# Performance work log

Measured on AMD Instinct MI355X. Metric: run time of the kernel, lower is better.

Reference implementation:

```python
import jax, jax.numpy as jnp
import numpy as np
import math

NUM_HEADS = 32
NUM_KV_HEADS = 8
HEAD_DIM = 128
ROPE_THETA = 10000.0


def _rope_cos_sin(position_ids, head_dim, dtype):
    # inv_freq: [head_dim/2]
    inv_freq = 1.0 / (ROPE_THETA ** (jnp.arange(0, head_dim, 2, dtype=jnp.float32) / head_dim))
    # freqs: [B, S, head_dim/2]
    freqs = position_ids.astype(jnp.float32)[:, :, None] * inv_freq[None, None, :]
    emb = jnp.concatenate([freqs, freqs], axis=-1)  # [B, S, head_dim]
    return jnp.cos(emb).astype(dtype), jnp.sin(emb).astype(dtype)


def _rotate_half(x):
    h = x.shape[-1] // 2
    return jnp.concatenate([-x[..., h:], x[..., :h]], axis=-1)


def setup_inputs() -> dict:
    key = jax.random.key(0)
    ks = jax.random.split(key, 5)
    B, S, H = 1, 2048, 4096
    kv_dim = NUM_KV_HEADS * HEAD_DIM
    return {
        "hidden_states": jax.random.normal(ks[0], (B, S, H), dtype=jnp.float32),
        "position_ids": jnp.arange(S, dtype=jnp.int64 if jax.config.jax_enable_x64 else jnp.int32)[None, :].repeat(B, axis=0),
        "Wq": jax.random.normal(ks[1], (H, H), dtype=jnp.float32) * 0.02,
        "Wk": jax.random.normal(ks[2], (kv_dim, H), dtype=jnp.float32) * 0.02,
        "Wv": jax.random.normal(ks[3], (kv_dim, H), dtype=jnp.float32) * 0.02,
        "Wo": jax.random.normal(ks[4], (H, H), dtype=jnp.float32) * 0.02,
    }


def reference(hidden_states, position_ids, Wq, Wk, Wv, Wo):
    B, S, H = hidden_states.shape
    groups = NUM_HEADS // NUM_KV_HEADS

    # QKV projections (nn.Linear: x @ W.T, no bias)
    q = (hidden_states @ Wq.T).reshape(B, S, NUM_HEADS, HEAD_DIM).transpose(0, 2, 1, 3)
    k = (hidden_states @ Wk.T).reshape(B, S, NUM_KV_HEADS, HEAD_DIM).transpose(0, 2, 1, 3)
    v = (hidden_states @ Wv.T).reshape(B, S, NUM_KV_HEADS, HEAD_DIM).transpose(0, 2, 1, 3)

    # RoPE
    cos, sin = _rope_cos_sin(position_ids, HEAD_DIM, q.dtype)
    cos = cos[:, None, :, :]  # [B,1,S,hd]
    sin = sin[:, None, :, :]
    q = q * cos + _rotate_half(q) * sin
    k = k * cos + _rotate_half(k) * sin

    # repeat_kv: expand KV heads to match Q heads
    k = jnp.repeat(k, groups, axis=1)  # [B, NUM_HEADS, S, hd]
    v = jnp.repeat(v, groups, axis=1)

    # scores + causal mask + fp32 softmax
    scores = jnp.einsum("bhqd,bhkd->bhqk", q, k) / math.sqrt(HEAD_DIM)
    causal = jnp.tril(jnp.ones((S, S), dtype=bool))
    scores = jnp.where(causal[None, None, :, :], scores, jnp.finfo(jnp.float32).min)
    attn = jax.nn.softmax(scores.astype(jnp.float32), axis=-1).astype(q.dtype)

    # attention output + output projection
    out = jnp.einsum("bhqk,bhkd->bhqd", attn, v)
    out = out.transpose(0, 2, 1, 3).reshape(B, S, H)
    return out @ Wo.T
```

## Files before the change

kernel.cpp:

```cpp
#include <hip/hip_runtime.h>
#include <stdint.h>


typedef __attribute__((ext_vector_type(8))) __bf16 bf16x8;
typedef __attribute__((ext_vector_type(4))) float floatx4;

#define S_LEN 2048
#define HID   4096
#define NH    32
#define NKV   8
#define HD    128

__device__ __forceinline__ unsigned short f2bf(float f) {
  union { float f; uint32_t u; } v; v.f = f;
  return (unsigned short)((v.u + 0x7fffu + ((v.u >> 16) & 1u)) >> 16);
}

__device__ __forceinline__ void gload_lds16(const unsigned short* g, unsigned short* l) {
  __builtin_amdgcn_global_load_lds(
      (const __attribute__((address_space(1))) void*)g,
      (__attribute__((address_space(3))) void*)l,
      16, 0, 0);
}

__global__ void cast_bf16_kernel(const float* __restrict__ in,
                                 unsigned short* __restrict__ out, int n4) {
  int i = blockIdx.x * blockDim.x + threadIdx.x;
  if (i >= n4) return;
  float4 f = ((const float4*)in)[i];
  ushort4 o = make_ushort4(f2bf(f.x), f2bf(f.y), f2bf(f.z), f2bf(f.w));
  ((ushort4*)out)[i] = o;
}

#define GT 32

__device__ __forceinline__ void read_frag4(
    bf16x8* f, const unsigned short* S, int row0, int l15, int quad) {
#pragma unroll
  for (int i = 0; i < 4; ++i) {
    const int row = row0 + i * 16 + l15;
    f[i] = *(const bf16x8*)&S[row * GT + (((quad ^ (row >> 1)) & 3) * 8)];
  }
}

__device__ __forceinline__ void mfma_c8(
    const bf16x8* a, const bf16x8* b, floatx4 acc[8][4], int mi0) {
#pragma unroll
  for (int mi = 0; mi < 2; ++mi)
#pragma unroll
    for (int ni = 0; ni < 4; ++ni)
      acc[mi0 + mi][ni] = __builtin_amdgcn_mfma_f32_16x16x32_bf16(
          a[mi], b[ni], acc[mi0 + mi][ni], 0, 0, 0);
}

__global__ __launch_bounds__(512, 2) void gemm_bt256_kernel(
    const unsigned short* __restrict__ A,
    const unsigned short* __restrict__ B,
    float* __restrict__ C, int M, int N, int K) {
  __shared__ unsigned short As[4][256 * GT];
  __shared__ unsigned short Bs[4][256 * GT];
  const int m0 = blockIdx.y * 256;
  const int n0 = blockIdx.x * 256;
  const int tid = threadIdx.x;
  const int lane = tid & 63;
  const int wv = tid >> 6;
  const int wr = wv >> 2;
  const int wc = wv & 3;
  const int l15 = lane & 15;
  const int quad = lane >> 4;

  const int ch0 = wv * 64 + lane;
  const int ch1 = ch0 + 512;
  const int cs0 = ch0 ^ ((ch0 >> 3) & 3);
  const int cs1 = ch1 ^ ((ch1 >> 3) & 3);
  const int r0s = cs0 >> 2, c0s = (cs0 & 3) * 8;
  const int r1s = cs1 >> 2, c1s = (cs1 & 3) * 8;

  floatx4 acc[8][4];
#pragma unroll
  for (int i = 0; i < 8; i++)
#pragma unroll
    for (int j = 0; j < 4; j++) acc[i][j] = (floatx4){0.f, 0.f, 0.f, 0.f};

  const int T = K / GT;

#define STAGE_T(kk0, s)                                                        \
  do {                                                                         \
    gload_lds16(A + (size_t)(m0 + r0s) * K + (kk0) + c0s, &As[s][ch0 * 8]);    \
    gload_lds16(A + (size_t)(m0 + r1s) * K + (kk0) + c1s, &As[s][ch1 * 8]);    \
    gload_lds16(B + (size_t)(n0 + r0s) * K + (kk0) + c0s, &Bs[s][ch0 * 8]);    \
    gload_lds16(B + (size_t)(n0 + r1s) * K + (kk0) + c1s, &Bs[s][ch1 * 8]);    \
  } while (0)

  STAGE_T(0, 0);
  STAGE_T(GT, 1);
  STAGE_T(2 * GT, 2);
  asm volatile("s_waitcnt vmcnt(4)" ::: "memory");
  __builtin_amdgcn_s_barrier();

  bf16x8 fA[12], fB[12];
  read_frag4(fA + 0, As[0], wr * 128, l15, quad);
  read_frag4(fA + 4, As[0], wr * 128 + 64, l15, quad);
  read_frag4(fA + 8, Bs[0], wc * 64, l15, quad);
  asm volatile("s_waitcnt lgkmcnt(0)" ::: "memory");
  __builtin_amdgcn_sched_barrier(0);

#define MCLUSTER(CUR, mi0)                                                     \
  __builtin_amdgcn_sched_barrier(0);                                           \
  __builtin_amdgcn_s_setprio(1);                                               \
  mfma_c8((CUR) + (mi0), (CUR) + 8, acc, (mi0));                               \
  __builtin_amdgcn_s_setprio(0);                                               \
  __builtin_amdgcn_sched_barrier(0);

#define BODY(tt, CUR, NXT)                                                     \
  do {                                                                         \
    const int t_ = (tt);                                                       \
    const int sl_ = (t_ + 1) & 3;                                              \
    const bool rd_ = (t_ + 1 < T);                                             \
    if (rd_) read_frag4((NXT) + 0, As[sl_], wr * 128, l15, quad);              \
    MCLUSTER(CUR, 0)                                                           \
    if (rd_) read_frag4((NXT) + 4, As[sl_], wr * 128 + 64, l15, quad);         \
    MCLUSTER(CUR, 2)                                                           \
    if (rd_) read_frag4((NXT) + 8, Bs[sl_], wc * 64, l15, quad);               \
    MCLUSTER(CUR, 4)                                                           \
    if (t_ + 3 < T) STAGE_T((t_ + 3) * GT, (t_ + 3) & 3);                      \
    MCLUSTER(CUR, 6)                                                           \
    asm volatile("s_waitcnt lgkmcnt(0)" ::: "memory");                         \
                  \
    if (t_ + 3 < T)      { asm volatile("s_waitcnt vmcnt(4)" ::: "memory"); }  \
    else if (t_ + 2 < T) { asm volatile("s_waitcnt vmcnt(0)" ::: "memory"); }  \
    __builtin_amdgcn_sched_barrier(0);                                         \
    __builtin_amdgcn_s_barrier();                                              \
  } while (0)

  for (int t = 0; t < T; t += 2) {
    BODY(t, fA, fB);
    BODY(t + 1, fB, fA);
  }
#undef BODY
#undef MCLUSTER
#undef STAGE_T

#pragma unroll
  for (int mi = 0; mi < 8; ++mi) {
    const int row = m0 + wr * 128 + mi * 16 + quad * 4;
#pragma unroll
    for (int ni = 0; ni < 4; ++ni) {
      const int col = n0 + wc * 64 + ni * 16 + l15;
#pragma unroll
      for (int r = 0; r < 4; ++r)
        C[(size_t)(row + r) * N + col] = acc[mi][ni][r];
    }
  }
}

#define BM 128
#define BN 128
#define BK 32

__global__ __launch_bounds__(256) void gemm_bt_kernel(
    const unsigned short* __restrict__ A,
    const unsigned short* __restrict__ B,
    float* __restrict__ C, int M, int N, int K) {
  __shared__ unsigned short As[BM * BK];
  __shared__ unsigned short Bs[BN * BK];
  const int m0 = blockIdx.y * BM;
  const int n0 = blockIdx.x * BN;
  const int tid = threadIdx.x;
  const int lane = tid & 63;
  const int l15 = lane & 15;
  const int quad = lane >> 4;
  const int w = tid >> 6;
  const int wm = (w >> 1) * 64;
  const int wn = (w & 1) * 64;

  floatx4 acc[4][4];
#pragma unroll
  for (int i = 0; i < 4; i++)
#pragma unroll
    for (int j = 0; j < 4; j++) acc[i][j] = (floatx4){0.f, 0.f, 0.f, 0.f};

  const int c0 = tid, c1 = tid + 256;
  const int r0 = c0 >> 2, o0 = (c0 & 3) * 8;
  const int r1 = c1 >> 2, o1 = (c1 & 3) * 8;

  for (int k0 = 0; k0 < K; k0 += BK) {
    __syncthreads();
    gload_lds16(A + (size_t)(m0 + r0) * K + k0 + o0, As + c0 * 8);
    gload_lds16(A + (size_t)(m0 + r1) * K + k0 + o1, As + c1 * 8);
    gload_lds16(B + (size_t)(n0 + r0) * K + k0 + o0, Bs + c0 * 8);
    gload_lds16(B + (size_t)(n0 + r1) * K + k0 + o1, Bs + c1 * 8);
    __syncthreads();

    bf16x8 a_frag[4], b_frag[4];
#pragma unroll
    for (int mt = 0; mt < 4; mt++)
      a_frag[mt] = *(const bf16x8*)&As[(wm + mt * 16 + l15) * BK + quad * 8];
#pragma unroll
    for (int nt = 0; nt < 4; nt++)
      b_frag[nt] = *(const bf16x8*)&Bs[(wn + nt * 16 + l15) * BK + quad * 8];
#pragma unroll
    for (int mt = 0; mt < 4; mt++)
#pragma unroll
      for (int nt = 0; nt < 4; nt++)
        acc[mt][nt] = __builtin_amdgcn_mfma_f32_16x16x32_bf16(
            a_frag[mt], b_frag[nt], acc[mt][nt], 0, 0, 0);
  }

#pragma unroll
  for (int mt = 0; mt < 4; mt++) {
#pragma unroll
    for (int nt = 0; nt < 4; nt++) {
      const int row = m0 + wm + mt * 16 + quad * 4;
      const int col = n0 + wn + nt * 16 + l15;
#pragma unroll
      for (int r = 0; r < 4; r++)
        C[(size_t)(row + r) * N + col] = acc[mt][nt][r];
    }
  }
}

__global__ void rope_kernel(const float* __restrict__ Cqkv,
                            const int* __restrict__ pos_ids,
                            unsigned short* __restrict__ Qb,
                            unsigned short* __restrict__ Kb) {
  int t = blockIdx.x * blockDim.x + threadIdx.x;
  int j = t & 63;
  int s = t >> 6;
  int hh = blockIdx.y;
  float pos = (float)pos_ids[s];
  float ang = pos * exp2f(-0.20762050593045222f * (float)j);
  float c = cosf(ang), sn = sinf(ang);
  if (hh < NH) {
    const float* row = Cqkv + (size_t)s * 6144 + hh * HD;
    float x1 = row[j], x2 = row[j + 64];
    unsigned short* q = Qb + ((size_t)hh * S_LEN + s) * HD;
    q[j]      = f2bf(x1 * c - x2 * sn);
    q[j + 64] = f2bf(x2 * c + x1 * sn);
  } else {
    int kh = hh - NH;
    const float* row = Cqkv + (size_t)s * 6144 + HID + kh * HD;
    float x1 = row[j], x2 = row[j + 64];
    unsigned short* k = Kb + ((size_t)kh * S_LEN + s) * HD;
    k[j]      = f2bf(x1 * c - x2 * sn);
    k[j + 64] = f2bf(x2 * c + x1 * sn);
  }
}

__global__ void vtrans_kernel(const float* __restrict__ Cqkv,
                              unsigned short* __restrict__ Vt) {
  int t = blockIdx.x * blockDim.x + threadIdx.x;
  int s = t & (S_LEN - 1);
  int d = (t >> 11) & (HD - 1);
  int kh = t >> 18;
  Vt[((size_t)kh * HD + d) * S_LEN + s] =
      f2bf(Cqkv[(size_t)s * 6144 + (HID + NKV * HD) + kh * HD + d]);
}

__global__ __launch_bounds__(256, 2) void flash_attn_kernel(
    const unsigned short* __restrict__ Qb, const unsigned short* __restrict__ Kb,
    const unsigned short* __restrict__ Vt, unsigned short* __restrict__ O) {
  __shared__ unsigned short Ks[2][64 * 128];
  __shared__ unsigned short Vs[2][128 * 64];
  __shared__ unsigned short Ps[4][2][16 * 64];
  const int qb = gridDim.x - 1 - blockIdx.x;
  const int q0 = qb * 128;
  const int h = blockIdx.y;
  const int kvh = h >> 2;
  const int tid = threadIdx.x;
  const int lane = tid & 63;
  const int w = tid >> 6;
  const int l15 = lane & 15;
  const int quad = lane >> 4;
  const int qlo = q0 + w * 32;

  const unsigned short* Qh = Qb + (size_t)h * S_LEN * HD;
  const unsigned short* Kh = Kb + (size_t)kvh * S_LEN * HD;
  const unsigned short* Vh = Vt + (size_t)kvh * HD * S_LEN;

  const int nkt = q0 / 64 + 2;

#pragma unroll
  for (int it = 0; it < 4; it++) {
    int c = tid + it * 256;
    int kr = c >> 4, kj = (c & 15) ^ (kr & 15);
    gload_lds16(Kh + (size_t)kr * HD + kj * 8, Ks[0] + c * 8);
    int vd = c >> 3, vj = (c & 7) ^ (vd & 7);
    gload_lds16(Vh + (size_t)vd * S_LEN + vj * 8, Vs[0] + c * 8);
  }

  bf16x8 q_frag[2][4];
#pragma unroll
  for (int mf = 0; mf < 2; mf++)
#pragma unroll
    for (int kk = 0; kk < 4; kk++)
      q_frag[mf][kk] = *(const bf16x8*)&Qh[(size_t)(qlo + mf * 16 + l15) * HD + kk * 32 + quad * 8];

  bf16x8 ones_frag;
  {
    union { unsigned short u; __bf16 b; } ov;
    ov.u = (l15 == 0) ? 0x3F80 : 0;
#pragma unroll
    for (int j = 0; j < 8; j++) ones_frag[j] = ov.b;
  }

  floatx4 o_acc[2][8];
  floatx4 o_l[2];
#pragma unroll
  for (int mf = 0; mf < 2; mf++) {
#pragma unroll
    for (int i = 0; i < 8; i++) o_acc[mf][i] = (floatx4){0.f, 0.f, 0.f, 0.f};
    o_l[mf] = (floatx4){0.f, 0.f, 0.f, 0.f};
  }
  const float SC2 = 0.12751738f;

  for (int kt = 0; kt < nkt; kt++) {
    const int kbase = kt * 64;
    const int buf = kt & 1;
    __syncthreads();

    if (kt + 1 < nkt) {
      const int kb2 = kbase + 64;
#pragma unroll
      for (int it = 0; it < 4; it++) {
        int c = tid + it * 256;
        int kr = c >> 4, kj = (c & 15) ^ (kr & 15);
        gload_lds16(Kh + (size_t)(kb2 + kr) * HD + kj * 8, Ks[buf ^ 1] + c * 8);
        int vd = c >> 3, vj = (c & 7) ^ (vd & 7);
        gload_lds16(Vh + (size_t)vd * S_LEN + kb2 + vj * 8, Vs[buf ^ 1] + c * 8);
      }
    }

    if (kbase <= qlo + 31) {
      floatx4 s_acc[2][4];
#pragma unroll
      for (int mf = 0; mf < 2; mf++)
#pragma unroll
        for (int nt = 0; nt < 4; nt++) s_acc[mf][nt] = (floatx4){0.f, 0.f, 0.f, 0.f};
#pragma unroll
      for (int kk = 0; kk < 4; kk++)
#pragma unroll
        for (int nt = 0; nt < 4; nt++) {
          bf16x8 k_frag = *(const bf16x8*)&Ks[buf][(nt * 16 + l15) * 128 + (((kk * 4 + quad) ^ l15) * 8)];
#pragma unroll
          for (int mf = 0; mf < 2; mf++)
            s_acc[mf][nt] = __builtin_amdgcn_mfma_f32_16x16x32_bf16(
                q_frag[mf][kk], k_frag, s_acc[mf][nt], 0, 0, 0);
        }

      const bool diag = (kbase + 63 > qlo);
#pragma unroll
      for (int mf = 0; mf < 2; mf++) {
#pragma unroll
        for (int nt = 0; nt < 4; nt++) {
          int kc = kbase + nt * 16 + l15;
          int qrow = qlo + mf * 16 + quad * 4;
          int chunk2 = nt * 2 + (l15 >> 3);
          int coff = l15 & 7;
#pragma unroll
          for (int r = 0; r < 4; r++) {
            float pv = exp2f(s_acc[mf][nt][r] * SC2);
            if (diag && kc > qrow + r) pv = 0.f;
            int row = quad * 4 + r;
            Ps[w][mf][row * 64 + ((chunk2 ^ (row & 7)) * 8) + coff] = f2bf(pv);
          }
        }
      }

#pragma unroll
      for (int kk2 = 0; kk2 < 2; kk2++) {
        bf16x8 p_frag[2];
#pragma unroll
        for (int mf = 0; mf < 2; mf++)
          p_frag[mf] = *(const bf16x8*)&Ps[w][mf][l15 * 64 + (((kk2 * 4 + quad) ^ (l15 & 7)) * 8)];
#pragma unroll
        for (int dt = 0; dt < 8; dt++) {
          bf16x8 v_frag = *(const bf16x8*)&Vs[buf][(dt * 16 + l15) * 64 + (((kk2 * 4 + quad) ^ (l15 & 7)) * 8)];
#pragma unroll
          for (int mf = 0; mf < 2; mf++)
            o_acc[mf][dt] = __builtin_amdgcn_mfma_f32_16x16x32_bf16(
                p_frag[mf], v_frag, o_acc[mf][dt], 0, 0, 0);
        }
#pragma unroll
        for (int mf = 0; mf < 2; mf++)
          o_l[mf] = __builtin_amdgcn_mfma_f32_16x16x32_bf16(
              p_frag[mf], ones_frag, o_l[mf], 0, 0, 0);
      }
    }
  }

#pragma unroll
  for (int mf = 0; mf < 2; mf++)
#pragma unroll
    for (int r = 0; r < 4; r++) {
      float lsum = __shfl(o_l[mf][r], lane & 48, 64);
      float inv = 1.f / lsum;
      int qr = qlo + mf * 16 + quad * 4 + r;
#pragma unroll
      for (int dt = 0; dt < 8; dt++)
        O[(size_t)qr * HID + h * HD + dt * 16 + l15] = f2bf(o_acc[mf][dt][r] * inv);
    }
}

extern "C" void kernel_launch(void* const* d_in, const int* in_sizes, int n_in,
                              void* d_out, int out_size, void* d_ws, size_t ws_size,
                              hipStream_t stream) {
  const float* hidden = (const float*)d_in[0];
  const int*   pos    = (const int*)d_in[1];
  const float* Wq     = (const float*)d_in[2];
  const float* Wk     = (const float*)d_in[3];
  const float* Wv     = (const float*)d_in[4];
  const float* Wo     = (const float*)d_in[5];

  char* ws = (char*)d_ws;
  size_t off = 0;
  unsigned short* h_b    = (unsigned short*)(ws + off); off += (size_t)S_LEN * HID * 2;
  unsigned short* Wqkv_b = (unsigned short*)(ws + off); off += (size_t)6144 * HID * 2;
  unsigned short* Wo_b   = (unsigned short*)(ws + off); off += (size_t)HID * HID * 2;
  float*          Cqkv   = (float*)(ws + off);          off += (size_t)S_LEN * 6144 * 4;
  unsigned short* Qb     = (unsigned short*)(ws + off); off += (size_t)NH * S_LEN * HD * 2;
  unsigned short* Kb     = (unsigned short*)(ws + off); off += (size_t)NKV * S_LEN * HD * 2;
  unsigned short* Vt     = (unsigned short*)(ws + off); off += (size_t)NKV * HD * S_LEN * 2;
  unsigned short* attn_b = (unsigned short*)Cqkv;

  cast_bf16_kernel<<<(S_LEN * HID / 4) / 256, 256, 0, stream>>>(hidden, h_b, S_LEN * HID / 4);
  cast_bf16_kernel<<<(HID * HID / 4) / 256, 256, 0, stream>>>(Wq, Wqkv_b, HID * HID / 4);
  cast_bf16_kernel<<<(1024 * HID / 4) / 256, 256, 0, stream>>>(Wk, Wqkv_b + (size_t)4096 * HID, 1024 * HID / 4);
  cast_bf16_kernel<<<(1024 * HID / 4) / 256, 256, 0, stream>>>(Wv, Wqkv_b + (size_t)5120 * HID, 1024 * HID / 4);
  cast_bf16_kernel<<<(HID * HID / 4) / 256, 256, 0, stream>>>(Wo, Wo_b, HID * HID / 4);

  gemm_bt256_kernel<<<dim3(6144 / 256, S_LEN / 256), 512, 0, stream>>>(h_b, Wqkv_b, Cqkv, S_LEN, 6144, HID);

  rope_kernel<<<dim3(S_LEN * 64 / 256, NH + NKV), 256, 0, stream>>>(Cqkv, pos, Qb, Kb);
  vtrans_kernel<<<(NKV * HD * S_LEN) / 256, 256, 0, stream>>>(Cqkv, Vt);

  flash_attn_kernel<<<dim3(S_LEN / 128, NH), 256, 0, stream>>>(Qb, Kb, Vt, attn_b);

  gemm_bt_kernel<<<dim3(HID / BN, S_LEN / BM), 256, 0, stream>>>(attn_b, Wo_b, (float*)d_out, S_LEN, HID, HID);
}
```

Measured before the change: 573.8 us.

## Replace output projection GEMM with 4-stage pipelined 256x128 swizzled kernel

Replaces the simple single-buffered 128x128 output-projection GEMM with a 256x128-tile kernel of 512 threads. It uses a 4-deep LDS ring fed by async global-to-LDS loads, XOR-swizzled LDS layout, register double-buffered fragments and prioritized MFMA clusters, mirroring the QKV GEMM. The aim is to hide global load latency and LDS bank conflicts that the old two-syncthreads-per-tile loop exposed. Grid shrinks to 256 blocks, which may leave some CUs underused.

After: 546.9 us. -4.7%, faster.

```diff
diff --git a/kernel.cpp b/kernel.cpp
--- a/kernel.cpp
+++ b/kernel.cpp
@@ -45,6 +45,16 @@
 
 __device__ __forceinline__ void mfma_c8(
     const bf16x8* a, const bf16x8* b, floatx4 acc[8][4], int mi0) {
+#pragma unroll
+  for (int mi = 0; mi < 2; ++mi)
+#pragma unroll
+    for (int ni = 0; ni < 4; ++ni)
+      acc[mi0 + mi][ni] = __builtin_amdgcn_mfma_f32_16x16x32_bf16(
+          a[mi], b[ni], acc[mi0 + mi][ni], 0, 0, 0);
+}
+
+__device__ __forceinline__ void mfma8_44(
+    const bf16x8* a, const bf16x8* b, floatx4 acc[4][4], int mi0) {
 #pragma unroll
   for (int mi = 0; mi < 2; ++mi)
 #pragma unroll
@@ -126,7 +136,6 @@
     if (t_ + 3 < T) STAGE_T((t_ + 3) * GT, (t_ + 3) & 3);                      \
     MCLUSTER(CUR, 6)                                                           \
     asm volatile("s_waitcnt lgkmcnt(0)" ::: "memory");                         \
-                  \
     if (t_ + 3 < T)      { asm volatile("s_waitcnt vmcnt(4)" ::: "memory"); }  \
     else if (t_ + 2 < T) { asm volatile("s_waitcnt vmcnt(0)" ::: "memory"); }  \
     __builtin_amdgcn_sched_barrier(0);                                         \
@@ -154,25 +163,31 @@
   }
 }
 
-#define BM 128
-#define BN 128
-#define BK 32
-
-__global__ __launch_bounds__(256) void gemm_bt_kernel(
+__global__ __launch_bounds__(512, 2) void gemm_bt_256x128_kernel(
     const unsigned short* __restrict__ A,
     const unsigned short* __restrict__ B,
     float* __restrict__ C, int M, int N, int K) {
-  __shared__ unsigned short As[BM * BK];
-  __shared__ unsigned short Bs[BN * BK];
-  const int m0 = blockIdx.y * BM;
-  const int n0 = blockIdx.x * BN;
+  __shared__ unsigned short As[4][256 * GT];
+  __shared__ unsigned short Bs[4][128 * GT];
+  const int m0 = blockIdx.y * 256;
+  const int n0 = blockIdx.x * 128;
   const int tid = threadIdx.x;
   const int lane = tid & 63;
+  const int wv = tid >> 6;
+  const int wr = wv >> 1;
+  const int wc = wv & 1;
   const int l15 = lane & 15;
   const int quad = lane >> 4;
-  const int w = tid >> 6;
-  const int wm = (w >> 1) * 64;
-  const int wn = (w & 1) * 64;
+
+  const int ch0 = wv * 64 + lane;
+  const int ch1 = ch0 + 512;
+  const int cs0 = ch0 ^ ((ch0 >> 3) & 3);
+  const int cs1 = ch1 ^ ((ch1 >> 3) & 3);
+  const int r0s = cs0 >> 2, c0s = (cs0 & 3) * 8;
+  const int r1s = cs1 >> 2, c1s = (cs1 & 3) * 8;
+  const int chb = tid;
+  const int csb = chb ^ ((chb >> 3) & 3);
+  const int rbs = csb >> 2, cbs = (csb & 3) * 8;
 
   floatx4 acc[4][4];
 #pragma unroll
@@ -180,42 +195,68 @@
 #pragma unroll
     for (int j = 0; j < 4; j++) acc[i][j] = (floatx4){0.f, 0.f, 0.f, 0.f};
 
-  const int c0 = tid, c1 = tid + 256;
-  const int r0 = c0 >> 2, o0 = (c0 & 3) * 8;
-  const int r1 = c1 >> 2, o1 = (c1 & 3) * 8;
-
-  for (int k0 = 0; k0 < K; k0 += BK) {
-    __syncthreads();
-    gload_lds16(A + (size_t)(m0 + r0) * K + k0 + o0, As + c0 * 8);
-    gload_lds16(A + (size_t)(m0 + r1) * K + k0 + o1, As + c1 * 8);
-    gload_lds16(B + (size_t)(n0 + r0) * K + k0 + o0, Bs + c0 * 8);
-    gload_lds16(B + (size_t)(n0 + r1) * K + k0 + o1, Bs + c1 * 8);
-    __syncthreads();
-
-    bf16x8 a_frag[4], b_frag[4];
-#pragma unroll
-    for (int mt = 0; mt < 4; mt++)
-      a_frag[mt] = *(const bf16x8*)&As[(wm + mt * 16 + l15) * BK + quad * 8];
-#pragma unroll
-    for (int nt = 0; nt < 4; nt++)
-      b_frag[nt] = *(const bf16x8*)&Bs[(wn + nt * 16 + l15) * BK + quad * 8];
-#pragma unroll
-    for (int mt = 0; mt < 4; mt++)
-#pragma unroll
-      for (int nt = 0; nt < 4; nt++)
-        acc[mt][nt] = __builtin_amdgcn_mfma_f32_16x16x32_bf16(
-            a_frag[mt], b_frag[nt], acc[mt][nt], 0, 0, 0);
-  }
-
-#pragma unroll
-  for (int mt = 0; mt < 4; mt++) {
-#pragma unroll
-    for (int nt = 0; nt < 4; nt++) {
-      const int row = m0 + wm + mt * 16 + quad * 4;
-      const int col = n0 + wn + nt * 16 + l15;
-#pragma unroll
-      for (int r = 0; r < 4; r++)
-        C[(size_t)(row + r) * N + col] = acc[mt][nt][r];
+  const int T = K / GT;
+
+#define STAGE_T(kk0, s)                                                        \
+  do {                                                                         \
+    gload_lds16(A + (size_t)(m0 + r0s) * K + (kk0) + c0s, &As[s][ch0 * 8]);    \
+    gload_lds16(A + (size_t)(m0 + r1s) * K + (kk0) + c1s, &As[s][ch1 * 8]);    \
+    gload_lds16(B + (size_t)(n0 + rbs) * K + (kk0) + cbs, &Bs[s][chb * 8]);    \
+  } while (0)
+
+  STAGE_T(0, 0);
+  STAGE_T(GT, 1);
+  STAGE_T(2 * GT, 2);
+  asm volatile("s_waitcnt vmcnt(3)" ::: "memory");
+  __builtin_amdgcn_s_barrier();
+
+  bf16x8 fA[8], fB[8];
+  read_frag4(fA + 0, As[0], wr * 64, l15, quad);
+  read_frag4(fA + 4, Bs[0], wc * 64, l15, quad);
+  asm volatile("s_waitcnt lgkmcnt(0)" ::: "memory");
+  __builtin_amdgcn_sched_barrier(0);
+
+#define MC8(CUR, mi0)                                                          \
+  __builtin_amdgcn_sched_barrier(0);                                           \
+  __builtin_amdgcn_s_setprio(1);                                               \
+  mfma8_44((CUR) + (mi0), (CUR) + 4, acc, (mi0));                              \
+  __builtin_amdgcn_s_setprio(0);                                               \
+  __builtin_amdgcn_sched_barrier(0);
+
+#define BODY(tt, CUR, NXT)                                                     \
+  do {                                                                         \
+    const int t_ = (tt);                                                       \
+    const int sl_ = (t_ + 1) & 3;                                              \
+    const bool rd_ = (t_ + 1 < T);                                             \
+    if (rd_) read_frag4((NXT) + 0, As[sl_], wr * 64, l15, quad);               \
+    MC8(CUR, 0)                                                                \
+    if (rd_) read_frag4((NXT) + 4, Bs[sl_], wc * 64, l15, quad);               \
+    if (t_ + 3 < T) STAGE_T((t_ + 3) * GT, (t_ + 3) & 3);                      \
+    MC8(CUR, 2)                                                                \
+    asm volatile("s_waitcnt lgkmcnt(0)" ::: "memory");                         \
+    if (t_ + 3 < T)      { asm volatile("s_waitcnt vmcnt(3)" ::: "memory"); }  \
+    else if (t_ + 2 < T) { asm volatile("s_waitcnt vmcnt(0)" ::: "memory"); }  \
+    __builtin_amdgcn_sched_barrier(0);                                         \
+    __builtin_amdgcn_s_barrier();                                              \
+  } while (0)
+
+  for (int t = 0; t < T; t += 2) {
+    BODY(t, fA, fB);
+    BODY(t + 1, fB, fA);
+  }
+#undef BODY
+#undef MC8
+#undef STAGE_T
+
+#pragma unroll
+  for (int mi = 0; mi < 4; ++mi) {
+    const int row = m0 + wr * 64 + mi * 16 + quad * 4;
+#pragma unroll
+    for (int ni = 0; ni < 4; ++ni) {
+      const int col = n0 + wc * 64 + ni * 16 + l15;
+#pragma unroll
+      for (int r = 0; r < 4; ++r)
+        C[(size_t)(row + r) * N + col] = acc[mi][ni][r];
     }
   }
 }
@@ -436,5 +477,5 @@
 
   flash_attn_kernel<<<dim3(S_LEN / 128, NH), 256, 0, stream>>>(Qb, Kb, Vt, attn_b);
 
-  gemm_bt_kernel<<<dim3(HID / BN, S_LEN / BM), 256, 0, stream>>>(attn_b, Wo_b, (float*)d_out, S_LEN, HID, HID);
-}
+  gemm_bt_256x128_kernel<<<dim3(HID / 128, S_LEN / 256), 512, 0, stream>>>(attn_b, Wo_b, (float*)d_out, S_LEN, HID, HID);
+}
```
